# Optimization experiments

Hardware: AMD Instinct MI355X
Metric: run time of the kernel (lower is better)

The kernel has to match this reference:

```python
import jax, jax.numpy as jnp
import numpy as np

B, H, W, CIN, C, L = 2, 512, 512, 64, 64, 4
TAU = 1.0


def _conv3x3(x, w):
    # NHWC input, HWIO kernel, SAME zero padding, stride 1 (SignalConv2D corr=True)
    return jax.lax.conv_general_dilated(
        x, w, window_strides=(1, 1), padding='SAME',
        dimension_numbers=('NHWC', 'HWIO', 'NHWC'))


def setup_inputs() -> dict:
    key = jax.random.key(0)
    ks = jax.random.split(key, 10)
    return {
        'x0': jax.random.normal(ks[0], (B, H, W, CIN), jnp.float32),
        'spa_mask': jax.random.uniform(ks[1], (B, H, W, 1), jnp.float32),
        'gumbel_u': jax.random.uniform(ks[2], (1, L, 2, C), jnp.float32),
        'ch_mask': jax.random.uniform(ks[3], (1, L, 2, C), jnp.float32),
        'w0': jax.random.normal(ks[4], (3, 3, CIN, C), jnp.float32) * 0.05,
        'w1': jax.random.normal(ks[5], (3, 3, C, C), jnp.float32) * 0.05,
        'w2': jax.random.normal(ks[6], (3, 3, C, C), jnp.float32) * 0.05,
        'w3': jax.random.normal(ks[7], (3, 3, C, C), jnp.float32) * 0.05,
        'w_collect': jax.random.normal(ks[8], (L * C, C), jnp.float32) * 0.05,
        'b_collect': jnp.zeros((C,), jnp.float32),
    }


def reference(x0, spa_mask, gumbel_u, ch_mask, w0, w1, w2, w3, w_collect, b_collect):
    # Gumbel-softmax channel routing mask over the {dense, sparse} axis (axis=2)
    g = -jnp.log(-jnp.log(jnp.clip(gumbel_u, 1e-10, 1.0)))
    ch = jax.nn.softmax((ch_mask + g) / TAU, axis=2)  # (1, L, 2, C)

    ws = [w0, w1, w2, w3]
    out_feats = []
    fea = x0
    for i in range(L):
        cd = ch[:, i, 0, :][:, None, None, :]  # dense-channel mask  (1,1,1,C)
        cs = ch[:, i, 1, :][:, None, None, :]  # sparse-channel mask (1,1,1,C)
        if i == 0:
            fea = _conv3x3(fea, ws[0])
            fea = fea * cs * spa_mask + fea * cd
        else:
            cdp = ch[:, i - 1, 0, :][:, None, None, :]
            csp = ch[:, i - 1, 1, :][:, None, None, :]
            fea_d = _conv3x3(fea * cdp, ws[i])
            fea_s = _conv3x3(fea * csp, ws[i])
            fea = (fea_d * cs * spa_mask + fea_d * cd
                   + fea_s * cs * spa_mask + fea_s * cd * spa_mask)
        fea = jax.nn.relu(fea)
        out_feats.append(fea)

    cat = jnp.concatenate(out_feats, axis=-1)  # (B, H, W, L*C)
    # 1x1 stride-1 Conv2DTranspose == pointwise linear + bias
    out = jnp.einsum('bhwi,io->bhwo', cat, w_collect) + b_collect
    return out, ch
```

## Files before the change

kernel.cpp:

```cpp
#include <hip/hip_runtime.h>
#include <hip/hip_fp16.h>

#define BB 2
#define HH 512
#define WW 512
#define CC 64
#define PW 514
#define PIMG (514*514)

typedef _Float16 f16;
typedef _Float16 f16x8 __attribute__((ext_vector_type(8)));
typedef _Float16 f16x4 __attribute__((ext_vector_type(4)));
typedef float f32x4 __attribute__((ext_vector_type(4)));

static __device__ __forceinline__ f16x8 zero_f16x8() {
    f16x8 z = {(f16)0,(f16)0,(f16)0,(f16)0,(f16)0,(f16)0,(f16)0,(f16)0};
    return z;
}

__global__ void k_prep_ch(const float* __restrict__ gum, const float* __restrict__ chm,
                          float* __restrict__ ws_ch, float* __restrict__ out_ch) {
    int t = threadIdx.x;
    int l = t >> 6, c = t & 63;
    float u0 = gum[(l*2+0)*64+c], u1 = gum[(l*2+1)*64+c];
    u0 = fminf(fmaxf(u0, 1e-10f), 1.0f);
    u1 = fminf(fmaxf(u1, 1e-10f), 1.0f);
    float a0 = chm[(l*2+0)*64+c] - logf(-logf(u0));
    float a1 = chm[(l*2+1)*64+c] - logf(-logf(u1));
    float m = fmaxf(a0, a1);
    float e0 = expf(a0-m), e1 = expf(a1-m);
    float s = e0 + e1;
    float c0 = e0/s, c1 = e1/s;
    ws_ch[(l*2+0)*64+c] = c0;  ws_ch[(l*2+1)*64+c] = c1;
    out_ch[(l*2+0)*64+c] = c0; out_ch[(l*2+1)*64+c] = c1;
}

__global__ void k_pack(const float* __restrict__ w0, const float* __restrict__ w1,
                       const float* __restrict__ w2, const float* __restrict__ w3,
                       const float* __restrict__ wc, const float* __restrict__ ch,
                       f16* __restrict__ bpk0, f16* __restrict__ bpkL, f16* __restrict__ wcpk) {
    int idx = blockIdx.x * 256 + threadIdx.x;
    if (idx < 36864) {
        int j = idx & 7, lane = (idx>>3)&63, nb = (idx>>9)&3, kb = idx>>11;
        int k = kb*32 + (lane>>4)*8 + j;
        int tap = k>>6, ci = k&63;
        int co = nb*16 + (lane&15);
        bpk0[idx] = (f16)w0[(tap*64+ci)*64+co];
    } else if (idx < 36864 + 221184) {
        int i2 = idx - 36864;
        int l = i2 / 73728;
        int r = i2 % 73728;
        int j = r&7, lane=(r>>3)&63, nb=(r>>9)&7, kb=r>>12;
        int k = kb*32 + (lane>>4)*8 + j;
        int tap = k>>6, ci = k&63;
        int copr = nb*16 + (lane&15);
        int co = copr & 63;
        const float* w = (l==0)? w1 : (l==1)? w2 : w3;
        float scale = (copr < 64) ? ch[(l*2+0)*64+ci] : ch[(l*2+1)*64+ci];
        bpkL[i2] = (f16)(w[(tap*64+ci)*64+co] * scale);
    } else if (idx < 36864 + 221184 + 16384) {
        int i3 = idx - (36864 + 221184);
        int j=i3&7, lane=(i3>>3)&63, nb=(i3>>9)&3, kb=(i3>>11)&1, l=i3>>12;
        int k = kb*32 + (lane>>4)*8 + j;
        int n = nb*16 + (lane&15);
        wcpk[i3] = (f16)wc[(l*64+k)*64+n];
    }
}

__global__ void k_guard(f16* __restrict__ buf) {
    int idx = blockIdx.x*256 + threadIdx.x;
    const int TOT = 2*2052*8;
    if (idx >= TOT) return;
    int c8 = idx & 7, g = idx >> 3;
    int b = g / 2052, r = g % 2052;
    int hp, wp;
    if      (r < 514)  { hp = 0;        wp = r; }
    else if (r < 1028) { hp = 513;      wp = r-514; }
    else if (r < 1540) { hp = r-1027;   wp = 0; }
    else               { hp = r-1539;   wp = 513; }
    *(f16x8*)(buf + ((size_t)(b*PW+hp)*PW + wp)*64 + c8*8) = zero_f16x8();
}

template<int MODE>
__global__ __launch_bounds__(256, 2) void k_conv(const void* __restrict__ in_, f16* __restrict__ out,
        const f16* __restrict__ bpk, const float* __restrict__ ch_l,
        const float* __restrict__ spa) {
    constexpr int NBT = (MODE==0) ? 4 : 8;
    constexpr int NF  = (MODE==0) ? 2 : 4;
    __shared__ f16 smem[4*136*64];
    const int wt = blockIdx.x, hb = blockIdx.y, b = blockIdx.z;
    const int h0 = hb*2;
    const int tid = threadIdx.x, lane = tid & 63, wid = tid >> 6;
    const int px0 = wt*128;
    const int sub  = lane & 7;
    const int srel = lane >> 3;
    const int cblk = sub ^ srel;

    if (MODE == 0) {
        const float* inF = (const float*)in_;
        #pragma unroll
        for (int half = 0; half < 2; ++half) {
            const int J0 = half ? 9 : 0;
            const int JN = half ? 8 : 9;
            f32x4 v0[9], v1[9];
            bool ok[9];
            int dst[9];
            #pragma unroll
            for (int t = 0; t < JN; ++t) {
                int j = (J0 + t)*4 + wid;
                int r = j / 17, i = j % 17;
                int s = i*8 + srel;
                int hin = h0 + r - 1;
                int win = px0 + s - 1;
                ok[t] = ((unsigned)hin < HH) && ((unsigned)win < WW);
                dst[t] = r*17408 + i*1024 + lane*16;
                if (ok[t]) {
                    const f32x4* p = (const f32x4*)(inF + (((size_t)(b*HH + hin)*WW + win)*CC + cblk*8));
                    v0[t] = p[0];
                    v1[t] = p[1];
                }
            }
            #pragma unroll
            for (int t = 0; t < JN; ++t) {
                f16x8 o = zero_f16x8();
                if (ok[t]) {
                    o[0]=(f16)v0[t][0]; o[1]=(f16)v0[t][1]; o[2]=(f16)v0[t][2]; o[3]=(f16)v0[t][3];
                    o[4]=(f16)v1[t][0]; o[5]=(f16)v1[t][1]; o[6]=(f16)v1[t][2]; o[7]=(f16)v1[t][3];
                }
                *(f16x8*)((char*)smem + dst[t]) = o;
            }
        }
        __syncthreads();
    } else {
        const f16* inH = (const f16*)in_;
        #pragma unroll
        for (int jj = 0; jj < 9; ++jj) {
            int j = jj*4 + wid;
            if (j < 34) {
                int r = j / 17, i = j % 17;
                int s = i*8 + srel;
                const f16* src = inH + ((size_t)(b*PW + h0 + r)*PW + (px0 + s))*64 + cblk*8;
                __builtin_amdgcn_global_load_lds(
                    (const __attribute__((address_space(1))) uint32_t*)src,
                    (__attribute__((address_space(3))) uint32_t*)
                        ((char*)smem + r*17408 + i*1024),
                    16, 0, 0);
            }
        }
        __syncthreads();
        #pragma unroll
        for (int jj = 0; jj < 9; ++jj) {
            int j = 34 + jj*4 + wid;
            if (j < 68) {
                int r = j / 17, i = j % 17;
                int s = i*8 + srel;
                const f16* src = inH + ((size_t)(b*PW + h0 + r)*PW + (px0 + s))*64 + cblk*8;
                __builtin_amdgcn_global_load_lds(
                    (const __attribute__((address_space(1))) uint32_t*)src,
                    (__attribute__((address_space(3))) uint32_t*)
                        ((char*)smem + r*17408 + i*1024),
                    16, 0, 0);
            }
        }
    }

    const int wr = wid >> 1, wn = wid & 1;
    const int lrow = lane & 15, q = lane >> 4;
    const char* smw = (const char*)smem + wr*17408;

    int sb[8][3], po[2][3];
    #pragma unroll
    for (int dxi = 0; dxi < 3; ++dxi) {
        int m7 = (lrow + dxi) & 7;
        po[0][dxi] = ((q)     ^ m7) * 16;
        po[1][dxi] = ((4 + q) ^ m7) * 16;
        #pragma unroll
        for (int mf = 0; mf < 8; ++mf)
            sb[mf][dxi] = (mf*16 + lrow + dxi) * 128;
    }

    f32x4 acc[8][NF];
    #pragma unroll
    for (int i=0;i<8;i++)
        #pragma unroll
        for (int j=0;j<NF;j++) { f32x4 z = {0.f,0.f,0.f,0.f}; acc[i][j] = z; }

    int nbIdx[4];
    nbIdx[0]=wn*2; nbIdx[1]=wn*2+1; nbIdx[2]=wn*2+4; nbIdx[3]=wn*2+5;

    const f16* blane = bpk + (size_t)lane*8;

    f16x8 acur[8], anxt[8], bcur[NF], bnxt[NF];
    #pragma unroll
    for (int nf=0; nf<NF; ++nf)
        bcur[nf] = *reinterpret_cast<const f16x8*>(blane + (size_t)nbIdx[nf]*512);
    #pragma unroll
    for (int mf=0; mf<8; ++mf)
        acur[mf] = *(const f16x8*)(smw + sb[mf][0] + po[0][0]);

    #pragma unroll
    for (int kb = 0; kb < 18; ++kb) {
        if (MODE == 1 && kb == 5) __syncthreads();
        if (kb < 17) {
            const int kn = kb + 1;
            const int rn = kn/6, dxin = (kn%6)/2, halfn = kn & 1;
            #pragma unroll
            for (int nf=0; nf<NF; ++nf)
                bnxt[nf] = *reinterpret_cast<const f16x8*>(blane + (size_t)(kn*NBT + nbIdx[nf])*512);
            #pragma unroll
            for (int mf=0; mf<8; ++mf)
                anxt[mf] = *(const f16x8*)(smw + rn*17408 + sb[mf][dxin] + po[halfn][dxin]);
        }
        __builtin_amdgcn_s_setprio(1);
        #pragma unroll
        for (int nf=0; nf<NF; ++nf) {
            #pragma unroll
            for (int mf=0; mf<8; ++mf)
                acc[mf][nf] = __builtin_amdgcn_mfma_f32_16x16x32_f16(acur[mf], bcur[nf], acc[mf][nf], 0,0,0);
        }
        __builtin_amdgcn_s_setprio(0);
        #pragma unroll
        for (int nf=0; nf<NF; ++nf) bcur[nf] = bnxt[nf];
        #pragma unroll
        for (int mf=0; mf<8; ++mf) acur[mf] = anxt[mf];
    }

    const float* cd = ch_l;
    const float* cs = ch_l + 64;
    const int h = h0 + wr;
    const size_t sparow = (size_t)(b*HH + h)*WW;
    const size_t outrow = (size_t)(b*PW + h + 1)*PW + 1;
    #pragma unroll
    for (int mf=0; mf<8; ++mf) {
        const int pixb = mf*16 + q*4;
        f32x4 sp4 = *(const f32x4*)(spa + sparow + px0 + pixb);
        float sp[4] = {sp4[0], sp4[1], sp4[2], sp4[3]};
        #pragma unroll
        for (int nf2=0; nf2<2; ++nf2) {
            int co = wn*32 + nf2*16 + lrow;
            float vcd = cd[co], vcs = cs[co];
            #pragma unroll
            for (int r=0; r<4; ++r) {
                float v;
                if (MODE==0) v = acc[mf][nf2][r] * (vcs*sp[r] + vcd);
                else         v = acc[mf][nf2][r] * (vcs*sp[r] + vcd) + acc[mf][nf2+2][r] * sp[r];
                v = fmaxf(v, 0.f);
                out[(outrow + px0 + pixb + r)*64 + co] = (f16)v;
            }
        }
    }
}

__global__ __launch_bounds__(256) void k_collect_all(
        const f16* __restrict__ f0, const f16* __restrict__ f1,
        const f16* __restrict__ f2, const f16* __restrict__ f3,
        const f16* __restrict__ wcpk, const float* __restrict__ bias,
        float* __restrict__ out) {
    const int wt = blockIdx.x, h = blockIdx.y, b = blockIdx.z;
    const int tid = threadIdx.x;
    const int lane = tid & 63, wid = tid >> 6;
    const int lrow = lane & 15, lk = (lane>>4)*8;
    const size_t inrow  = (size_t)(b*PW + h + 1)*PW + 1;
    const size_t outrow = (size_t)(b*HH + h)*WW;
    const int px0 = wt*256 + wid*64;

    const f16* feas[4] = {f0, f1, f2, f3};

    f32x4 acc[4][4];
    #pragma unroll
    for (int i=0;i<4;i++)
        #pragma unroll
        for (int j=0;j<4;j++) { f32x4 z = {0.f,0.f,0.f,0.f}; acc[i][j] = z; }

    f16x8 a_cur[4], a_nxt[4];
    #pragma unroll
    for (int mf=0; mf<4; ++mf)
        a_cur[mf] = *reinterpret_cast<const f16x8*>(f0 + (inrow + px0 + mf*16 + lrow)*64 + lk);

    #pragma unroll
    for (int kb=0; kb<8; ++kb) {
        if (kb < 7) {
            const f16* fl = feas[(kb+1)>>1];
            #pragma unroll
            for (int mf=0; mf<4; ++mf)
                a_nxt[mf] = *reinterpret_cast<const f16x8*>(fl + (inrow + px0 + mf*16 + lrow)*64 + ((kb+1)&1)*32 + lk);
        }
        #pragma unroll
        for (int nf=0; nf<4; ++nf) {
            f16x8 bb = *reinterpret_cast<const f16x8*>(wcpk + ((size_t)(kb*4 + nf)*64 + lane)*8);
            #pragma unroll
            for (int mf=0; mf<4; ++mf)
                acc[mf][nf] = __builtin_amdgcn_mfma_f32_16x16x32_f16(bb, a_cur[mf], acc[mf][nf], 0,0,0);
        }
        #pragma unroll
        for (int mf=0; mf<4; ++mf) a_cur[mf] = a_nxt[mf];
    }
    const int q = lane >> 4;
    #pragma unroll
    for (int mf=0; mf<4; ++mf) {
        const int pix = px0 + mf*16 + lrow;
        float* orow = out + (outrow + pix)*CC;
        #pragma unroll
        for (int nf=0; nf<4; ++nf) {
            const int co0 = nf*16 + q*4;
            f32x4 b4 = *(const f32x4*)(bias + co0);
            *(f32x4*)(orow + co0) = acc[mf][nf] + b4;
        }
    }
}

template<bool FIRST>
__global__ __launch_bounds__(256) void k_collect(const f16* __restrict__ fea,
        const f16* __restrict__ wcpk_l, const float* __restrict__ bias,
        float* __restrict__ out) {
    const int wt = blockIdx.x, h = blockIdx.y, b = blockIdx.z;
    const int tid = threadIdx.x;
    const int lane = tid & 63, wid = tid >> 6;
    const int lrow = lane & 15, lk = (lane>>4)*8;
    const size_t inrow  = (size_t)(b*PW + h + 1)*PW + 1;
    const size_t outrow = (size_t)(b*HH + h)*WW;
    const int px0 = wt*64 + wid*16;

    f32x4 acc[4];
    #pragma unroll
    for (int j=0;j<4;j++) { f32x4 z = {0.f,0.f,0.f,0.f}; acc[j] = z; }

    #pragma unroll
    for (int kb=0; kb<2; ++kb) {
        f16x8 a = *reinterpret_cast<const f16x8*>(fea + (inrow + px0 + lrow)*64 + kb*32 + lk);
        #pragma unroll
        for (int nf=0; nf<4; ++nf) {
            f16x8 bb = *reinterpret_cast<const f16x8*>(wcpk_l + ((size_t)(kb*4 + nf)*64 + lane)*8);
            acc[nf] = __builtin_amdgcn_mfma_f32_16x16x32_f16(bb, a, acc[nf], 0,0,0);
        }
    }
    const int q = lane >> 4;
    const int pix = px0 + lrow;
    float* orow = out + (outrow + pix)*CC;
    #pragma unroll
    for (int nf=0; nf<4; ++nf) {
        const int co0 = nf*16 + q*4;
        f32x4 v = acc[nf];
        #pragma unroll
        for (int r=0;r<4;++r) {
            float x = v[r];
            if (FIRST) x += bias[co0+r];
            else       x += orow[co0+r];
            orow[co0+r] = x;
        }
    }
}

extern "C" void kernel_launch(void* const* d_in, const int* in_sizes, int n_in,
                              void* d_out, int out_size, void* d_ws, size_t ws_size,
                              hipStream_t stream) {
    const float* x0  = (const float*)d_in[0];
    const float* spa = (const float*)d_in[1];
    const float* gum = (const float*)d_in[2];
    const float* chm = (const float*)d_in[3];
    const float* w0  = (const float*)d_in[4];
    const float* w1  = (const float*)d_in[5];
    const float* w2  = (const float*)d_in[6];
    const float* w3  = (const float*)d_in[7];
    const float* wc  = (const float*)d_in[8];
    const float* bias= (const float*)d_in[9];
    float* out = (float*)d_out;

    char* ws = (char*)d_ws;
    const size_t WBASE = (1u<<20);
    const size_t FB = 67699712ull;
    const size_t NEED_A = WBASE + 4*FB;
    const size_t NEED_B = WBASE + 2*FB;
    if (ws_size < NEED_B) return;

    float* ws_ch = (float*)ws;
    f16* bpk0 = (f16*)(ws + 4096);
    f16* bpkL = (f16*)(ws + 4096 + 73728);
    f16* wcpk = (f16*)(ws + 4096 + 73728 + 442368);

    k_prep_ch<<<1, 256, 0, stream>>>(gum, chm, ws_ch, out + 33554432);
    k_pack<<<1072, 256, 0, stream>>>(w0, w1, w2, w3, wc, ws_ch, bpk0, bpkL, wcpk);

    dim3 gcv(4, 256, 2);
    dim3 gca(2, 512, 2);
    dim3 gcf(8, 512, 2);

    if (ws_size >= NEED_A) {
        f16* R0 = (f16*)(ws + WBASE);
        f16* R1 = (f16*)(ws + WBASE + FB);
        f16* R2 = (f16*)(ws + WBASE + 2*FB);
        f16* R3 = (f16*)(ws + WBASE + 3*FB);
        k_guard<<<129, 256, 0, stream>>>(R1);
        k_guard<<<129, 256, 0, stream>>>(R2);
        k_guard<<<129, 256, 0, stream>>>(R3);
        k_conv<0><<<gcv, 256, 0, stream>>>(x0, R1, bpk0,          ws_ch + 0,   spa);
        k_conv<1><<<gcv, 256, 0, stream>>>(R1, R2, bpkL + 0,      ws_ch + 128, spa);
        k_conv<1><<<gcv, 256, 0, stream>>>(R2, R3, bpkL + 73728,  ws_ch + 256, spa);
        k_conv<1><<<gcv, 256, 0, stream>>>(R3, R0, bpkL + 147456, ws_ch + 384, spa);
        k_collect_all<<<gca, 256, 0, stream>>>(R1, R2, R3, R0, wcpk, bias, out);
    } else {
        f16* P0 = (f16*)(ws + WBASE);
        f16* P1 = (f16*)(ws + WBASE + FB);
        k_guard<<<129, 256, 0, stream>>>(P0);
        k_guard<<<129, 256, 0, stream>>>(P1);
        k_conv<0><<<gcv, 256, 0, stream>>>(x0, P1, bpk0,          ws_ch + 0,   spa);
        k_collect<true ><<<gcf, 256, 0, stream>>>(P1, wcpk + 0,     bias, out);
        k_conv<1><<<gcv, 256, 0, stream>>>(P1, P0, bpkL + 0,      ws_ch + 128, spa);
        k_collect<false><<<gcf, 256, 0, stream>>>(P0, wcpk + 4096,  bias, out);
        k_conv<1><<<gcv, 256, 0, stream>>>(P0, P1, bpkL + 73728,  ws_ch + 256, spa);
        k_collect<false><<<gcf, 256, 0, stream>>>(P1, wcpk + 8192,  bias, out);
        k_conv<1><<<gcv, 256, 0, stream>>>(P1, P0, bpkL + 147456, ws_ch + 384, spa);
        k_collect<false><<<gcf, 256, 0, stream>>>(P0, wcpk + 12288, bias, out);
    }
}
```

Baseline: 358.2 us.

## Pipeline input row loads with MFMA compute in first conv layer

```diff
diff --git a/kernel.cpp b/kernel.cpp
--- a/kernel.cpp
+++ b/kernel.cpp
@@ -16,6 +16,13 @@
 static __device__ __forceinline__ f16x8 zero_f16x8() {
     f16x8 z = {(f16)0,(f16)0,(f16)0,(f16)0,(f16)0,(f16)0,(f16)0,(f16)0};
     return z;
+}
+
+static __device__ __forceinline__ f16x8 cvt_pair(f32x4 a, f32x4 b) {
+    f16x8 o;
+    o[0]=(f16)a[0]; o[1]=(f16)a[1]; o[2]=(f16)a[2]; o[3]=(f16)a[3];
+    o[4]=(f16)b[0]; o[5]=(f16)b[1]; o[6]=(f16)b[2]; o[7]=(f16)b[3];
+    return o;
 }
 
 __global__ void k_prep_ch(const float* __restrict__ gum, const float* __restrict__ chm,
@@ -96,41 +103,60 @@
     const int srel = lane >> 3;
     const int cblk = sub ^ srel;
 
+    const float* inF = (const float*)in_;
+
+    f32x4 v0c[5], v1c[5], v0d[5], v1d[5];
+    bool okc[5], okd[5];
+    int dstc[5], dstd[5];
+
     if (MODE == 0) {
-        const float* inF = (const float*)in_;
-        #pragma unroll
-        for (int half = 0; half < 2; ++half) {
-            const int J0 = half ? 9 : 0;
-            const int JN = half ? 8 : 9;
+        {
             f32x4 v0[9], v1[9];
             bool ok[9];
             int dst[9];
             #pragma unroll
-            for (int t = 0; t < JN; ++t) {
-                int j = (J0 + t)*4 + wid;
-                int r = j / 17, i = j % 17;
+            for (int t = 0; t < 9; ++t) {
+                int j = t*4 + wid;
+                ok[t] = false;
+                if (j < 34) {
+                    int r = j / 17, i = j % 17;
+                    int s = i*8 + srel;
+                    int hin = h0 + r - 1, win = px0 + s - 1;
+                    ok[t] = ((unsigned)hin < HH) && ((unsigned)win < WW);
+                    dst[t] = r*17408 + i*1024 + lane*16;
+                    if (ok[t]) {
+                        const f32x4* p = (const f32x4*)(inF + (((size_t)(b*HH + hin)*WW + win)*CC + cblk*8));
+                        v0[t] = p[0];
+                        v1[t] = p[1];
+                    }
+                }
+            }
+            #pragma unroll
+            for (int t = 0; t < 9; ++t) {
+                if (t*4 + wid < 34) {
+                    f16x8 o = ok[t] ? cvt_pair(v0[t], v1[t]) : zero_f16x8();
+                    *(f16x8*)((char*)smem + dst[t]) = o;
+                }
+            }
+        }
+        __syncthreads();
+        #pragma unroll
+        for (int t = 0; t < 5; ++t) {
+            int i = t*4 + wid;
+            okc[t] = false;
+            if (i < 17) {
                 int s = i*8 + srel;
-                int hin = h0 + r - 1;
                 int win = px0 + s - 1;
-                ok[t] = ((unsigned)hin < HH) && ((unsigned)win < WW);
-                dst[t] = r*17408 + i*1024 + lane*16;
-                if (ok[t]) {
-                    const f32x4* p = (const f32x4*)(inF + (((size_t)(b*HH + hin)*WW + win)*CC + cblk*8));
-                    v0[t] = p[0];
-                    v1[t] = p[1];
-                }
-            }
-            #pragma unroll
-            for (int t = 0; t < JN; ++t) {
-                f16x8 o = zero_f16x8();
-                if (ok[t]) {
-                    o[0]=(f16)v0[t][0]; o[1]=(f16)v0[t][1]; o[2]=(f16)v0[t][2]; o[3]=(f16)v0[t][3];
-                    o[4]=(f16)v1[t][0]; o[5]=(f16)v1[t][1]; o[6]=(f16)v1[t][2]; o[7]=(f16)v1[t][3];
-                }
-                *(f16x8*)((char*)smem + dst[t]) = o;
-            }
-        }
-        __syncthreads();
+                okc[t] = (unsigned)win < WW;
+                dstc[t] = 2*17408 + i*1024 + lane*16;
+                if (okc[t]) {
+                    const f32x4* p = (const f32x4*)(inF + (((size_t)(b*HH + h0 + 1)*WW + win)*CC + cblk*8));
+                    v0c[t] = p[0];
+                    v1c[t] = p[1];
+                }
+            }
+        }
+        __builtin_amdgcn_sched_barrier(0);
     } else {
         const f16* inH = (const f16*)in_;
         #pragma unroll
@@ -200,7 +226,45 @@
 
     #pragma unroll
     for (int kb = 0; kb < 18; ++kb) {
-        if (MODE == 1 && kb == 5) __syncthreads();
+        if (kb == 5) {
+            if (MODE == 0) {
+                #pragma unroll
+                for (int t = 0; t < 5; ++t) {
+                    if (t*4 + wid < 17) {
+                        f16x8 o = okc[t] ? cvt_pair(v0c[t], v1c[t]) : zero_f16x8();
+                        *(f16x8*)((char*)smem + dstc[t]) = o;
+                    }
+                }
+                #pragma unroll
+                for (int t = 0; t < 5; ++t) {
+                    int i = t*4 + wid;
+                    okd[t] = false;
+                    if (i < 17) {
+                        int s = i*8 + srel;
+                        int hin = h0 + 2, win = px0 + s - 1;
+                        okd[t] = ((unsigned)hin < HH) && ((unsigned)win < WW);
+                        dstd[t] = 3*17408 + i*1024 + lane*16;
+                        if (okd[t]) {
+                            const f32x4* p = (const f32x4*)(inF + (((size_t)(b*HH + hin)*WW + win)*CC + cblk*8));
+                            v0d[t] = p[0];
+                            v1d[t] = p[1];
+                        }
+                    }
+                }
+                __builtin_amdgcn_sched_barrier(0);
+            }
+            __syncthreads();
+        }
+        if (MODE == 0 && kb == 11) {
+            #pragma unroll
+            for (int t = 0; t < 5; ++t) {
+                if (t*4 + wid < 17) {
+                    f16x8 o = okd[t] ? cvt_pair(v0d[t], v1d[t]) : zero_f16x8();
+                    *(f16x8*)((char*)smem + dstd[t]) = o;
+                }
+            }
+            __syncthreads();
+        }
         if (kb < 17) {
             const int kn = kb + 1;
             const int rn = kn/6, dxin = (kn%6)/2, halfn = kn & 1;
```

After: 357.6 us. About the same (-0.2%).
